# Kernel tuning notes

Hardware: AMD Instinct MI355X
Metric: run time of the kernel (lower is better)

Reference implementation:

```python
import jax, jax.numpy as jnp
import numpy as np

B, N, DIM = 32, 3136, 64
H, DH, AGENTS = 8, 8, 49
INNER = H * DH  # 64
SCALE = DH ** -0.5


def setup_inputs() -> dict:
    key = jax.random.key(0)
    ks = jax.random.split(key, 7)
    s = 0.05
    return {
        "x1": jax.random.normal(ks[0], (B, N, DIM), jnp.float32),
        "x2": jax.random.normal(ks[1], (B, N, INNER), jnp.float32),
        "Wq": jax.random.normal(ks[2], (INNER, DIM), jnp.float32) * s,   # to_q (out,in)
        "Wk": jax.random.normal(ks[3], (DIM, INNER), jnp.float32) * s,   # to_k
        "Wv": jax.random.normal(ks[4], (DIM, INNER), jnp.float32) * s,   # to_v
        "Wo": jax.random.normal(ks[5], (2 * DIM, 2 * DIM), jnp.float32) * s,  # to_out linear
        "bo": jax.random.normal(ks[6], (2 * DIM,), jnp.float32) * s,
    }


def _split_heads(t):
    # (b, n, h*d) -> (b, h, n, d)
    b, n, hd = t.shape
    return t.reshape(b, n, H, hd // H).transpose(0, 2, 1, 3)


def reference(x1, x2, Wq, Wk, Wv, Wo, bo):
    b, n, _ = x1.shape
    q = x1 @ Wq.T                      # (b, n, 64)
    k = x2 @ Wk.T                      # (b, n, dim=64)
    v = x2 @ Wv.T
    # AdaptiveAvgPool2d((49, dim)): n % 49 == 0 and channel 64->64 is identity,
    # so pooling is an exact block mean over the sequence axis.
    agent = q.reshape(b, AGENTS, n // AGENTS, q.shape[-1]).mean(axis=2)  # (b, 49, 64)

    agent_h = _split_heads(agent)      # (b, h, 49, d)
    q1 = _split_heads(q)               # (b, h, n, d)
    k_h = _split_heads(k)
    v_h = _split_heads(v)

    # stage 0: agent tokens attend over keys/values (dropout is identity at eval)
    dots0 = jnp.einsum('bhid,bhjd->bhij', agent_h, k_h) * SCALE   # (b,h,49,n)
    attn0 = jax.nn.softmax(dots0, axis=-1)
    out0 = jnp.einsum('bhij,bhjd->bhid', attn0, v_h)              # (b,h,49,d)

    # stage 1: queries attend over agent tokens
    dots1 = jnp.einsum('bhid,bhjd->bhij', q1, agent_h) * SCALE    # (b,h,n,49)
    attn1 = jax.nn.softmax(dots1, axis=-1)
    out1 = jnp.einsum('bhij,bhjd->bhid', attn1, out0)             # (b,h,n,d)

    out1 = out1.transpose(0, 2, 1, 3).reshape(b, n, -1)           # (b,n,64)
    out1 = jnp.concatenate([out1, x1], axis=-1)                   # (b,n,128)
    return out1 @ Wo.T + bo
```

## Files before the change

kernel.cpp:

```cpp
#include <hip/hip_runtime.h>
#include <hip/hip_bf16.h>

#define NB 32
#define NSEQ 3136
#define NDIM 64
#define NH 8
#define NAG 49

static constexpr float kScale = 0.35355339059327378f;
static constexpr float kLog2e = 1.4426950408889634f;

typedef unsigned short us;
typedef __attribute__((ext_vector_type(8))) __bf16 bf16x8;
typedef __attribute__((ext_vector_type(4))) __bf16 bf16x4;
typedef __attribute__((ext_vector_type(2))) _Float16 f16x2;
typedef __attribute__((ext_vector_type(4))) _Float16 f16x4;
typedef __attribute__((ext_vector_type(8))) _Float16 f16x8;
typedef __attribute__((ext_vector_type(4))) float f32x4;

__device__ __forceinline__ float fexp2(float x) {
#if __has_builtin(__builtin_amdgcn_exp2f)
  return __builtin_amdgcn_exp2f(x);
#else
  return exp2f(x);
#endif
}

__device__ __forceinline__ float frcp(float x) {
#if __has_builtin(__builtin_amdgcn_rcpf)
  return __builtin_amdgcn_rcpf(x);
#else
  return 1.f / x;
#endif
}

__device__ __forceinline__ unsigned pk2(float a, float b) {
#if __has_builtin(__builtin_amdgcn_cvt_pkrtz)
  return __builtin_bit_cast(unsigned, __builtin_amdgcn_cvt_pkrtz(a, b));
#else
  f16x2 v = {(_Float16)a, (_Float16)b};
  return __builtin_bit_cast(unsigned, v);
#endif
}

__device__ __forceinline__ bf16x8 ldw8(const float* W, int row, int c0, int ld) {
  const float4* p = (const float4*)(W + (size_t)row * ld + c0);
  float4 v0 = p[0], v1 = p[1];
  bf16x8 r;
  r[0]=(__bf16)v0.x; r[1]=(__bf16)v0.y; r[2]=(__bf16)v0.z; r[3]=(__bf16)v0.w;
  r[4]=(__bf16)v1.x; r[5]=(__bf16)v1.y; r[6]=(__bf16)v1.z; r[7]=(__bf16)v1.w;
  return r;
}

__global__ __launch_bounds__(256) void agent_x1_kernel(
    const float* __restrict__ x1, const float* __restrict__ Wq,
    us* __restrict__ x1bf, us* __restrict__ agf16) {
  __shared__ float red[4][64];
  __shared__ float marr[64];
  const int a = blockIdx.x, b = blockIdx.y, t = threadIdx.x;
  const int i64 = t & 63, cb = t >> 6;

  {
    const float4* s1 = (const float4*)(x1 + ((size_t)(b * NSEQ) + a * 64 + i64) * NDIM + cb * 16);
    float4 v0 = s1[0], v1 = s1[1], v2 = s1[2], v3 = s1[3];
    bf16x8 p0, p1;
    p0[0]=(__bf16)v0.x; p0[1]=(__bf16)v0.y; p0[2]=(__bf16)v0.z; p0[3]=(__bf16)v0.w;
    p0[4]=(__bf16)v1.x; p0[5]=(__bf16)v1.y; p0[6]=(__bf16)v1.z; p0[7]=(__bf16)v1.w;
    p1[0]=(__bf16)v2.x; p1[1]=(__bf16)v2.y; p1[2]=(__bf16)v2.z; p1[3]=(__bf16)v2.w;
    p1[4]=(__bf16)v3.x; p1[5]=(__bf16)v3.y; p1[6]=(__bf16)v3.z; p1[7]=(__bf16)v3.w;
    __bf16* dst = (__bf16*)x1bf;
    *(bf16x8*)(dst + ((((size_t)b * NAG + a) * 8 + cb * 2) * 64 + i64) * 8) = p0;
    *(bf16x8*)(dst + ((((size_t)b * NAG + a) * 8 + cb * 2 + 1) * 64 + i64) * 8) = p1;
  }
  {
    const float* xc = x1 + ((size_t)(b * NSEQ) + a * 64 + cb * 16) * NDIM + i64;
    float cs = 0.f;
#pragma unroll
    for (int i = 0; i < 16; ++i) cs += xc[i * NDIM];
    red[cb][i64] = cs;
  }
  __syncthreads();
  if (t < 64) marr[t] = red[0][t] + red[1][t] + red[2][t] + red[3][t];
  __syncthreads();
  if (t < 64) {
    const float4* wqr = (const float4*)(Wq + (size_t)t * NDIM);
    const float4* mm = (const float4*)marr;
    float s0 = 0.f;
#pragma unroll
    for (int i = 0; i < 16; ++i) {
      float4 wv4 = wqr[i], m4 = mm[i];
      s0 += wv4.x * m4.x + wv4.y * m4.y + wv4.z * m4.z + wv4.w * m4.w;
    }
    const float val = s0 * (kScale * kLog2e / 64.f);
    ((_Float16*)agf16)[(((size_t)b * NH + (t >> 3)) * NAG + a) * 8 + (t & 7)] =
        (_Float16)val;
  }
}

__global__ __launch_bounds__(256) void kv_stage0_kernel(
    const float* __restrict__ x2, const float* __restrict__ Wk,
    const float* __restrict__ Wv, const us* __restrict__ agf16,
    float* __restrict__ pvp) {
  __shared__ __align__(16) __bf16 xb[64][72];
  __shared__ __align__(16) _Float16 klds[4][64][24];
  __shared__ __align__(16) _Float16 vlds[4][18][72];
  __shared__ __align__(16) _Float16 plds[4][64][40];
  const int a = blockIdx.x, b = blockIdx.y, t = threadIdx.x;
  const int i64 = t & 63, cb = t >> 6;
  const int w = cb, lr = (t >> 4) & 3, lc = t & 15;

  bf16x8 ak0 = ldw8(Wk, w * 16 + lc, lr * 8, NDIM);
  bf16x8 ak1 = ldw8(Wk, w * 16 + lc, 32 + lr * 8, NDIM);
  bf16x8 av0 = ldw8(Wv, w * 16 + lc, lr * 8, NDIM);
  bf16x8 av1 = ldw8(Wv, w * 16 + lc, 32 + lr * 8, NDIM);

  {
    const float4* s2 = (const float4*)(x2 + ((size_t)(b * NSEQ) + a * 64 + i64) * NDIM + cb * 16);
    float4 v0 = s2[0], v1 = s2[1], v2 = s2[2], v3 = s2[3];
    bf16x8 p0, p1;
    p0[0]=(__bf16)v0.x; p0[1]=(__bf16)v0.y; p0[2]=(__bf16)v0.z; p0[3]=(__bf16)v0.w;
    p0[4]=(__bf16)v1.x; p0[5]=(__bf16)v1.y; p0[6]=(__bf16)v1.z; p0[7]=(__bf16)v1.w;
    p1[0]=(__bf16)v2.x; p1[1]=(__bf16)v2.y; p1[2]=(__bf16)v2.z; p1[3]=(__bf16)v2.w;
    p1[4]=(__bf16)v3.x; p1[5]=(__bf16)v3.y; p1[6]=(__bf16)v3.z; p1[7]=(__bf16)v3.w;
    *(bf16x8*)&xb[i64][cb * 16] = p0; *(bf16x8*)&xb[i64][cb * 16 + 8] = p1;
  }
  __syncthreads();

  f32x4 acck[4], accv[4];
#pragma unroll
  for (int i = 0; i < 4; ++i) {
    acck[i] = (f32x4){0.f, 0.f, 0.f, 0.f};
    accv[i] = (f32x4){0.f, 0.f, 0.f, 0.f};
  }
#pragma unroll
  for (int nt = 0; nt < 4; ++nt) {
    bf16x8 x0 = *(const bf16x8*)&xb[nt * 16 + lc][lr * 8];
    bf16x8 x1f = *(const bf16x8*)&xb[nt * 16 + lc][32 + lr * 8];
    acck[nt] = __builtin_amdgcn_mfma_f32_16x16x32_bf16(ak0, x0, acck[nt], 0, 0, 0);
    acck[nt] = __builtin_amdgcn_mfma_f32_16x16x32_bf16(ak1, x1f, acck[nt], 0, 0, 0);
    accv[nt] = __builtin_amdgcn_mfma_f32_16x16x32_bf16(av0, x0, accv[nt], 0, 0, 0);
    accv[nt] = __builtin_amdgcn_mfma_f32_16x16x32_bf16(av1, x1f, accv[nt], 0, 0, 0);
  }
#pragma unroll
  for (int nt = 0; nt < 4; ++nt) {
    f16x4 pk4;
    pk4[0]=(_Float16)acck[nt][0]; pk4[1]=(_Float16)acck[nt][1];
    pk4[2]=(_Float16)acck[nt][2]; pk4[3]=(_Float16)acck[nt][3];
    *(f16x4*)&klds[w][nt * 16 + lc][lr * 4] = pk4;
#pragma unroll
    for (int j = 0; j < 4; ++j)
      vlds[w][lr * 4 + j][nt * 16 + lc] = (_Float16)accv[nt][j];
  }
  vlds[w][16][i64] = (_Float16)1.0f;

  const size_t bh0 = (size_t)b * NH + 2 * w;
  f16x8 ba[2][4];
#pragma unroll
  for (int hh = 0; hh < 2; ++hh)
#pragma unroll
    for (int at = 0; at < 4; ++at) {
      f16x8 v = (f16x8)(_Float16)0.0f;
      if (lr == 0) {
        int row = at * 16 + lc; if (row > 48) row = 48;
        v = *(const f16x8*)(agf16 + (bh0 + hh) * (NAG * 8) + row * 8);
      }
      ba[hh][at] = v;
    }

#pragma unroll
  for (int hh = 0; hh < 2; ++hh) {
    f32x4 accPV[4];
#pragma unroll
    for (int i = 0; i < 4; ++i) accPV[i] = (f32x4){0.f, 0.f, 0.f, 0.f};
#pragma unroll
    for (int half = 0; half < 2; ++half) {
#pragma unroll
      for (int tb = 0; tb < 2; ++tb) {
        const int tokbase = half * 32 + tb * 16;
        f16x8 kf = *(const f16x8*)&klds[w][tokbase + lc][hh * 8];
#pragma unroll
        for (int at = 0; at < 4; ++at) {
          f32x4 sc = __builtin_amdgcn_mfma_f32_16x16x32_f16(
              kf, ba[hh][at], (f32x4){0.f, 0.f, 0.f, 0.f}, 0, 0, 0);
          unsigned u0 = pk2(fexp2(sc[0]), fexp2(sc[1]));
          unsigned u1 = pk2(fexp2(sc[2]), fexp2(sc[3]));
          unsigned long long q = ((unsigned long long)u1 << 32) | u0;
          *(unsigned long long*)&plds[w][at * 16 + lc][tb * 16 + lr * 4] = q;
        }
      }
      const int frow = (lc < 8) ? hh * 8 + lc : 16;
      f16x8 vf = *(const f16x8*)&vlds[w][frow][half * 32 + lr * 8];
#pragma unroll
      for (int at = 0; at < 4; ++at) {
        f16x8 pf = *(const f16x8*)&plds[w][at * 16 + lc][lr * 8];
        accPV[at] = __builtin_amdgcn_mfma_f32_16x16x32_f16(pf, vf, accPV[at], 0, 0, 0);
      }
    }
    if (lc < 9) {
      float* dst = pvp + ((size_t)a * (NB * NH) + bh0 + hh) * 441;
#pragma unroll
      for (int at = 0; at < 4; ++at)
#pragma unroll
        for (int j = 0; j < 4; ++j) {
          const int ag = at * 16 + lr * 4 + j;
          if (ag < NAG) dst[ag * 9 + lc] = accPV[at][j];
        }
    }
  }
}

__global__ __launch_bounds__(256) void aofin_kernel(
    const float* __restrict__ pvp, us* __restrict__ pvtF) {
  __shared__ float acc[441];
  const int h = blockIdx.x, b = blockIdx.y, t = threadIdx.x;
  const size_t bh = (size_t)b * NH + h;
  for (int s = t; s < 441; s += 256) {
    float v = 0.f;
#pragma unroll 7
    for (int aa = 0; aa < NAG; ++aa)
      v += pvp[((size_t)aa * (NB * NH) + bh) * 441 + s];
    acc[s] = v;
  }
  __syncthreads();
  if (t < 64) {
    us* col = pvtF + bh * 1024 + t;
    float inv = (t < NAG) ? frcp(acc[t * 9 + 8]) : 0.f;
#pragma unroll
    for (int f = 0; f < 8; ++f) {
      float val = (t < NAG) ? acc[t * 9 + f] * inv : 0.f;
      _Float16 hv = (_Float16)val;
      col[f * 64] = __builtin_bit_cast(us, hv);
    }
    col[8 * 64] = (t < NAG) ? (us)0x3C00 : (us)0;
#pragma unroll
    for (int f = 9; f < 16; ++f) col[f * 64] = 0;
  }
}

__global__ __launch_bounds__(512, 8) void stage1_out_kernel(
    const us* __restrict__ x1bf, const float* __restrict__ Wq,
    const us* __restrict__ agf16, const us* __restrict__ pvtF,
    const float* __restrict__ Wo, const float* __restrict__ bo,
    float* __restrict__ out) {
  __shared__ __align__(16) __bf16 xa[64][72];
  __shared__ __align__(16) us qcat[64][72];
  __shared__ __align__(16) _Float16 pW[8][16][72];
  const int tile = blockIdx.x, b = blockIdx.y;
  const int t = threadIdx.x, tokl = t & 63, h = t >> 6;
  const int w = h, lane = t & 63, lr = (lane >> 4) & 3, lc = lane & 15;
  const int mtile = w & 3, thalf = w >> 2;
  const size_t bh = (size_t)b * NH + w;

  bf16x8 wqf0 = ldw8(Wq, mtile * 16 + lc, lr * 8, NDIM);
  bf16x8 wqf1 = ldw8(Wq, mtile * 16 + lc, 32 + lr * 8, NDIM);

  f16x8 ba[4];
#pragma unroll
  for (int at = 0; at < 4; ++at) {
    f16x8 v = (f16x8)(_Float16)0.0f;
    if (lr == 0) {
      int row = at * 16 + lc; if (row > 48) row = 48;
      v = *(const f16x8*)(agf16 + bh * (NAG * 8) + row * 8);
    }
    ba[at] = v;
  }
  const us* pvb = pvtF + bh * 1024;
  f16x8 pvB0 = *(const f16x8*)(pvb + lc * 64 + lr * 8);
  f16x8 pvB1 = *(const f16x8*)(pvb + lc * 64 + 32 + lr * 8);

  {
    bf16x8 p = *(const bf16x8*)((const __bf16*)x1bf +
        ((((size_t)b * NAG + tile) * 8 + h) * 64 + tokl) * 8);
    *(bf16x8*)&xa[tokl][h * 8] = p;
  }
  __syncthreads();

  {
    f32x4 aq[2];
    aq[0] = (f32x4){0.f,0.f,0.f,0.f}; aq[1] = (f32x4){0.f,0.f,0.f,0.f};
#pragma unroll
    for (int nt = 0; nt < 2; ++nt) {
      bf16x8 bx0 = *(const bf16x8*)&xa[thalf * 32 + nt * 16 + lc][lr * 8];
      bf16x8 bx1 = *(const bf16x8*)&xa[thalf * 32 + nt * 16 + lc][32 + lr * 8];
      aq[nt] = __builtin_amdgcn_mfma_f32_16x16x32_bf16(wqf0, bx0, aq[nt], 0, 0, 0);
      aq[nt] = __builtin_amdgcn_mfma_f32_16x16x32_bf16(wqf1, bx1, aq[nt], 0, 0, 0);
    }
#pragma unroll
    for (int nt = 0; nt < 2; ++nt) {
      f16x4 pk;
      pk[0]=(_Float16)aq[nt][0]; pk[1]=(_Float16)aq[nt][1];
      pk[2]=(_Float16)aq[nt][2]; pk[3]=(_Float16)aq[nt][3];
      *(f16x4*)&qcat[thalf * 32 + nt * 16 + lc][mtile * 16 + lr * 4] = pk;
    }
  }
  __syncthreads();

  {
    _Float16* psw = &pW[w][0][0];
#pragma unroll 1
    for (int g = 0; g < 4; ++g) {
      f16x8 qf = *(const f16x8*)&qcat[g * 16 + lc][w * 8];
#pragma unroll
      for (int at = 0; at < 4; ++at) {
        f32x4 sc = __builtin_amdgcn_mfma_f32_16x16x32_f16(
            ba[at], qf, (f32x4){0.f, 0.f, 0.f, 0.f}, 0, 0, 0);
        unsigned u0 = pk2(fexp2(sc[0]), fexp2(sc[1]));
        unsigned u1 = pk2(fexp2(sc[2]), fexp2(sc[3]));
        unsigned long long qq = ((unsigned long long)u1 << 32) | u0;
        *(unsigned long long*)&psw[(size_t)lc * 72 + at * 16 + lr * 4] = qq;
      }
      f16x8 pA0 = *(const f16x8*)&psw[(size_t)lc * 72 + lr * 8];
      f16x8 pA1 = *(const f16x8*)&psw[(size_t)lc * 72 + 32 + lr * 8];
      f32x4 pv = __builtin_amdgcn_mfma_f32_16x16x32_f16(
          pvB0, pA0, (f32x4){0.f, 0.f, 0.f, 0.f}, 0, 0, 0);
      pv = __builtin_amdgcn_mfma_f32_16x16x32_f16(pvB1, pA1, pv, 0, 0, 0);
      float den = __shfl(pv[0], 32 + lc);
      float inv = frcp(den);
      if (lr < 2) {
        bf16x4 pc;
        pc[0] = (__bf16)(pv[0] * inv); pc[1] = (__bf16)(pv[1] * inv);
        pc[2] = (__bf16)(pv[2] * inv); pc[3] = (__bf16)(pv[3] * inv);
        *(bf16x4*)((__bf16*)&qcat[g * 16 + lc][0] + w * 8 + lr * 4) = pc;
      }
    }
  }
  bf16x8 wof[4];
#pragma unroll
  for (int ks = 0; ks < 4; ++ks)
    wof[ks] = ldw8(Wo, w * 16 + lc, ks * 32 + lr * 8, 128);
  f32x4 bv = *(const f32x4*)(bo + w * 16 + lr * 4);
  __syncthreads();

  {
    f32x4 acc[4];
#pragma unroll
    for (int i = 0; i < 4; ++i) acc[i] = (f32x4){0.f,0.f,0.f,0.f};
#pragma unroll
    for (int ks = 0; ks < 4; ++ks) {
#pragma unroll
      for (int nt = 0; nt < 4; ++nt) {
        bf16x8 bx = (ks < 2) ? *(const bf16x8*)&qcat[nt * 16 + lc][ks * 32 + lr * 8]
                             : *(const bf16x8*)&xa[nt * 16 + lc][(ks - 2) * 32 + lr * 8];
        acc[nt] = __builtin_amdgcn_mfma_f32_16x16x32_bf16(wof[ks], bx, acc[nt], 0, 0, 0);
      }
    }
#pragma unroll
    for (int nt = 0; nt < 4; ++nt) {
      f32x4 v = acc[nt] + bv;
      float* dst = out + ((size_t)b * NSEQ + tile * 64 + nt * 16 + lc) * 128 + w * 16 + lr * 4;
      *(f32x4*)dst = v;
    }
  }
}

extern "C" void kernel_launch(void* const* d_in, const int* in_sizes, int n_in,
                              void* d_out, int out_size, void* d_ws, size_t ws_size,
                              hipStream_t stream) {
  (void)in_sizes; (void)n_in; (void)out_size; (void)ws_size;
  const float* x1 = (const float*)d_in[0];
  const float* x2 = (const float*)d_in[1];
  const float* Wq = (const float*)d_in[2];
  const float* Wk = (const float*)d_in[3];
  const float* Wv = (const float*)d_in[4];
  const float* Wo = (const float*)d_in[5];
  const float* bo = (const float*)d_in[6];
  float* out = (float*)d_out;

  us* x1bf = (us*)d_ws;
  us* agf16 = x1bf + (size_t)NB * NSEQ * 64;
  float* pvp = (float*)(agf16 + (size_t)NB * NH * NAG * 8);
  us* pvtF = (us*)(pvp + (size_t)NAG * NB * NH * 441);

  agent_x1_kernel<<<dim3(NAG, NB), 256, 0, stream>>>(x1, Wq, x1bf, agf16);
  kv_stage0_kernel<<<dim3(NAG, NB), 256, 0, stream>>>(x2, Wk, Wv, agf16, pvp);
  aofin_kernel<<<dim3(NH, NB), 256, 0, stream>>>(pvp, pvtF);
  stage1_out_kernel<<<dim3(NAG, NB), 512, 0, stream>>>(x1bf, Wq, agf16,
                                                       pvtF, Wo, bo, out);
}
```

Measured before the change: 79.31 us.

## Process two sequence chunks per stage0 block and store fp16 partials

Each stage0 block now handles two 64-token chunks, accumulating PV partials across both in registers, which halves the number of partial rows written and read by the reduction kernel. Partials are also stored as fp16 instead of fp32, and the layout is changed to contiguous per (b,h). This cuts the workspace traffic between stage0 and aofin but halves the grid size of stage0 and adds fp16 rounding to the unnormalized softmax sums, which risks overflow or precision loss.

```diff
diff --git a/kernel.cpp b/kernel.cpp
--- a/kernel.cpp
+++ b/kernel.cpp
@@ -6,6 +6,7 @@
 #define NDIM 64
 #define NH 8
 #define NAG 49
+#define NPAIR 25
 
 static constexpr float kScale = 0.35355339059327378f;
 static constexpr float kLog2e = 1.4426950408889634f;
@@ -100,12 +101,12 @@
 __global__ __launch_bounds__(256) void kv_stage0_kernel(
     const float* __restrict__ x2, const float* __restrict__ Wk,
     const float* __restrict__ Wv, const us* __restrict__ agf16,
-    float* __restrict__ pvp) {
+    us* __restrict__ pvp) {
   __shared__ __align__(16) __bf16 xb[64][72];
   __shared__ __align__(16) _Float16 klds[4][64][24];
   __shared__ __align__(16) _Float16 vlds[4][18][72];
   __shared__ __align__(16) _Float16 plds[4][64][40];
-  const int a = blockIdx.x, b = blockIdx.y, t = threadIdx.x;
+  const int pair = blockIdx.x, b = blockIdx.y, t = threadIdx.x;
   const int i64 = t & 63, cb = t >> 6;
   const int w = cb, lr = (t >> 4) & 3, lc = t & 15;
 
@@ -113,45 +114,6 @@
   bf16x8 ak1 = ldw8(Wk, w * 16 + lc, 32 + lr * 8, NDIM);
   bf16x8 av0 = ldw8(Wv, w * 16 + lc, lr * 8, NDIM);
   bf16x8 av1 = ldw8(Wv, w * 16 + lc, 32 + lr * 8, NDIM);
-
-  {
-    const float4* s2 = (const float4*)(x2 + ((size_t)(b * NSEQ) + a * 64 + i64) * NDIM + cb * 16);
-    float4 v0 = s2[0], v1 = s2[1], v2 = s2[2], v3 = s2[3];
-    bf16x8 p0, p1;
-    p0[0]=(__bf16)v0.x; p0[1]=(__bf16)v0.y; p0[2]=(__bf16)v0.z; p0[3]=(__bf16)v0.w;
-    p0[4]=(__bf16)v1.x; p0[5]=(__bf16)v1.y; p0[6]=(__bf16)v1.z; p0[7]=(__bf16)v1.w;
-    p1[0]=(__bf16)v2.x; p1[1]=(__bf16)v2.y; p1[2]=(__bf16)v2.z; p1[3]=(__bf16)v2.w;
-    p1[4]=(__bf16)v3.x; p1[5]=(__bf16)v3.y; p1[6]=(__bf16)v3.z; p1[7]=(__bf16)v3.w;
-    *(bf16x8*)&xb[i64][cb * 16] = p0; *(bf16x8*)&xb[i64][cb * 16 + 8] = p1;
-  }
-  __syncthreads();
-
-  f32x4 acck[4], accv[4];
-#pragma unroll
-  for (int i = 0; i < 4; ++i) {
-    acck[i] = (f32x4){0.f, 0.f, 0.f, 0.f};
-    accv[i] = (f32x4){0.f, 0.f, 0.f, 0.f};
-  }
-#pragma unroll
-  for (int nt = 0; nt < 4; ++nt) {
-    bf16x8 x0 = *(const bf16x8*)&xb[nt * 16 + lc][lr * 8];
-    bf16x8 x1f = *(const bf16x8*)&xb[nt * 16 + lc][32 + lr * 8];
-    acck[nt] = __builtin_amdgcn_mfma_f32_16x16x32_bf16(ak0, x0, acck[nt], 0, 0, 0);
-    acck[nt] = __builtin_amdgcn_mfma_f32_16x16x32_bf16(ak1, x1f, acck[nt], 0, 0, 0);
-    accv[nt] = __builtin_amdgcn_mfma_f32_16x16x32_bf16(av0, x0, accv[nt], 0, 0, 0);
-    accv[nt] = __builtin_amdgcn_mfma_f32_16x16x32_bf16(av1, x1f, accv[nt], 0, 0, 0);
-  }
-#pragma unroll
-  for (int nt = 0; nt < 4; ++nt) {
-    f16x4 pk4;
-    pk4[0]=(_Float16)acck[nt][0]; pk4[1]=(_Float16)acck[nt][1];
-    pk4[2]=(_Float16)acck[nt][2]; pk4[3]=(_Float16)acck[nt][3];
-    *(f16x4*)&klds[w][nt * 16 + lc][lr * 4] = pk4;
-#pragma unroll
-    for (int j = 0; j < 4; ++j)
-      vlds[w][lr * 4 + j][nt * 16 + lc] = (_Float16)accv[nt][j];
-  }
-  vlds[w][16][i64] = (_Float16)1.0f;
 
   const size_t bh0 = (size_t)b * NH + 2 * w;
   f16x8 ba[2][4];
@@ -166,59 +128,112 @@
       }
       ba[hh][at] = v;
     }
+  vlds[w][16][i64] = (_Float16)1.0f;
+
+  f32x4 accPV[2][4];
+#pragma unroll
+  for (int hh = 0; hh < 2; ++hh)
+#pragma unroll
+    for (int i = 0; i < 4; ++i) accPV[hh][i] = (f32x4){0.f, 0.f, 0.f, 0.f};
+
+  for (int cc = 0; cc < 2; ++cc) {
+    const int a = pair * 2 + cc;
+    if (a >= NAG) break;
+    if (cc) __syncthreads();
+
+    {
+      const float4* s2 = (const float4*)(x2 + ((size_t)(b * NSEQ) + a * 64 + i64) * NDIM + cb * 16);
+      float4 v0 = s2[0], v1 = s2[1], v2 = s2[2], v3 = s2[3];
+      bf16x8 p0, p1;
+      p0[0]=(__bf16)v0.x; p0[1]=(__bf16)v0.y; p0[2]=(__bf16)v0.z; p0[3]=(__bf16)v0.w;
+      p0[4]=(__bf16)v1.x; p0[5]=(__bf16)v1.y; p0[6]=(__bf16)v1.z; p0[7]=(__bf16)v1.w;
+      p1[0]=(__bf16)v2.x; p1[1]=(__bf16)v2.y; p1[2]=(__bf16)v2.z; p1[3]=(__bf16)v2.w;
+      p1[4]=(__bf16)v3.x; p1[5]=(__bf16)v3.y; p1[6]=(__bf16)v3.z; p1[7]=(__bf16)v3.w;
+      *(bf16x8*)&xb[i64][cb * 16] = p0; *(bf16x8*)&xb[i64][cb * 16 + 8] = p1;
+    }
+    __syncthreads();
+
+    f32x4 acck[4], accv[4];
+#pragma unroll
+    for (int i = 0; i < 4; ++i) {
+      acck[i] = (f32x4){0.f, 0.f, 0.f, 0.f};
+      accv[i] = (f32x4){0.f, 0.f, 0.f, 0.f};
+    }
+#pragma unroll
+    for (int nt = 0; nt < 4; ++nt) {
+      bf16x8 x0 = *(const bf16x8*)&xb[nt * 16 + lc][lr * 8];
+      bf16x8 x1f = *(const bf16x8*)&xb[nt * 16 + lc][32 + lr * 8];
+      acck[nt] = __builtin_amdgcn_mfma_f32_16x16x32_bf16(ak0, x0, acck[nt], 0, 0, 0);
+      acck[nt] = __builtin_amdgcn_mfma_f32_16x16x32_bf16(ak1, x1f, acck[nt], 0, 0, 0);
+      accv[nt] = __builtin_amdgcn_mfma_f32_16x16x32_bf16(av0, x0, accv[nt], 0, 0, 0);
+      accv[nt] = __builtin_amdgcn_mfma_f32_16x16x32_bf16(av1, x1f, accv[nt], 0, 0, 0);
+    }
+#pragma unroll
+    for (int nt = 0; nt < 4; ++nt) {
+      f16x4 pk4;
+      pk4[0]=(_Float16)acck[nt][0]; pk4[1]=(_Float16)acck[nt][1];
+      pk4[2]=(_Float16)acck[nt][2]; pk4[3]=(_Float16)acck[nt][3];
+      *(f16x4*)&klds[w][nt * 16 + lc][lr * 4] = pk4;
+#pragma unroll
+      for (int j = 0; j < 4; ++j)
+        vlds[w][lr * 4 + j][nt * 16 + lc] = (_Float16)accv[nt][j];
+    }
+
+#pragma unroll
+    for (int hh = 0; hh < 2; ++hh) {
+#pragma unroll
+      for (int half = 0; half < 2; ++half) {
+#pragma unroll
+        for (int tb = 0; tb < 2; ++tb) {
+          const int tokbase = half * 32 + tb * 16;
+          f16x8 kf = *(const f16x8*)&klds[w][tokbase + lc][hh * 8];
+#pragma unroll
+          for (int at = 0; at < 4; ++at) {
+            f32x4 sc = __builtin_amdgcn_mfma_f32_16x16x32_f16(
+                kf, ba[hh][at], (f32x4){0.f, 0.f, 0.f, 0.f}, 0, 0, 0);
+            unsigned u0 = pk2(fexp2(sc[0]), fexp2(sc[1]));
+            unsigned u1 = pk2(fexp2(sc[2]), fexp2(sc[3]));
+            unsigned long long q = ((unsigned long long)u1 << 32) | u0;
+            *(unsigned long long*)&plds[w][at * 16 + lc][tb * 16 + lr * 4] = q;
+          }
+        }
+        const int frow = (lc < 8) ? hh * 8 + lc : 16;
+        f16x8 vf = *(const f16x8*)&vlds[w][frow][half * 32 + lr * 8];
+#pragma unroll
+        for (int at = 0; at < 4; ++at) {
+          f16x8 pf = *(const f16x8*)&plds[w][at * 16 + lc][lr * 8];
+          accPV[hh][at] =
+              __builtin_amdgcn_mfma_f32_16x16x32_f16(pf, vf, accPV[hh][at], 0, 0, 0);
+        }
+      }
+    }
+  }
 
 #pragma unroll
   for (int hh = 0; hh < 2; ++hh) {
-    f32x4 accPV[4];
-#pragma unroll
-    for (int i = 0; i < 4; ++i) accPV[i] = (f32x4){0.f, 0.f, 0.f, 0.f};
-#pragma unroll
-    for (int half = 0; half < 2; ++half) {
-#pragma unroll
-      for (int tb = 0; tb < 2; ++tb) {
-        const int tokbase = half * 32 + tb * 16;
-        f16x8 kf = *(const f16x8*)&klds[w][tokbase + lc][hh * 8];
-#pragma unroll
-        for (int at = 0; at < 4; ++at) {
-          f32x4 sc = __builtin_amdgcn_mfma_f32_16x16x32_f16(
-              kf, ba[hh][at], (f32x4){0.f, 0.f, 0.f, 0.f}, 0, 0, 0);
-          unsigned u0 = pk2(fexp2(sc[0]), fexp2(sc[1]));
-          unsigned u1 = pk2(fexp2(sc[2]), fexp2(sc[3]));
-          unsigned long long q = ((unsigned long long)u1 << 32) | u0;
-          *(unsigned long long*)&plds[w][at * 16 + lc][tb * 16 + lr * 4] = q;
-        }
-      }
-      const int frow = (lc < 8) ? hh * 8 + lc : 16;
-      f16x8 vf = *(const f16x8*)&vlds[w][frow][half * 32 + lr * 8];
-#pragma unroll
-      for (int at = 0; at < 4; ++at) {
-        f16x8 pf = *(const f16x8*)&plds[w][at * 16 + lc][lr * 8];
-        accPV[at] = __builtin_amdgcn_mfma_f32_16x16x32_f16(pf, vf, accPV[at], 0, 0, 0);
-      }
-    }
     if (lc < 9) {
-      float* dst = pvp + ((size_t)a * (NB * NH) + bh0 + hh) * 441;
+      _Float16* dst = (_Float16*)pvp + ((bh0 + hh) * NPAIR + pair) * 441;
 #pragma unroll
       for (int at = 0; at < 4; ++at)
 #pragma unroll
         for (int j = 0; j < 4; ++j) {
           const int ag = at * 16 + lr * 4 + j;
-          if (ag < NAG) dst[ag * 9 + lc] = accPV[at][j];
+          if (ag < NAG) dst[ag * 9 + lc] = (_Float16)accPV[hh][at][j];
         }
     }
   }
 }
 
 __global__ __launch_bounds__(256) void aofin_kernel(
-    const float* __restrict__ pvp, us* __restrict__ pvtF) {
+    const us* __restrict__ pvp, us* __restrict__ pvtF) {
   __shared__ float acc[441];
   const int h = blockIdx.x, b = blockIdx.y, t = threadIdx.x;
   const size_t bh = (size_t)b * NH + h;
+  const _Float16* src = (const _Float16*)pvp + bh * (NPAIR * 441);
   for (int s = t; s < 441; s += 256) {
     float v = 0.f;
-#pragma unroll 7
-    for (int aa = 0; aa < NAG; ++aa)
-      v += pvp[((size_t)aa * (NB * NH) + bh) * 441 + s];
+#pragma unroll 5
+    for (int p = 0; p < NPAIR; ++p) v += (float)src[(size_t)p * 441 + s];
     acc[s] = v;
   }
   __syncthreads();
@@ -368,11 +383,11 @@
 
   us* x1bf = (us*)d_ws;
   us* agf16 = x1bf + (size_t)NB * NSEQ * 64;
-  float* pvp = (float*)(agf16 + (size_t)NB * NH * NAG * 8);
-  us* pvtF = (us*)(pvp + (size_t)NAG * NB * NH * 441);
+  us* pvp = agf16 + (size_t)NB * NH * NAG * 8;
+  us* pvtF = pvp + (size_t)NB * NH * NPAIR * 441;
 
   agent_x1_kernel<<<dim3(NAG, NB), 256, 0, stream>>>(x1, Wq, x1bf, agf16);
-  kv_stage0_kernel<<<dim3(NAG, NB), 256, 0, stream>>>(x2, Wk, Wv, agf16, pvp);
+  kv_stage0_kernel<<<dim3(NPAIR, NB), 256, 0, stream>>>(x2, Wk, Wv, agf16, pvp);
   aofin_kernel<<<dim3(NH, NB), 256, 0, stream>>>(pvp, pvtF);
   stage1_out_kernel<<<dim3(NAG, NB), 512, 0, stream>>>(x1bf, Wq, agf16,
                                                        pvtF, Wo, bo, out);
```

Result: faster. 76.37 us (-3.7%).
